# Optimization experiments

Measured on AMD Instinct MI355X. Metric: run time of the kernel, lower is better.

## Reference

```python
import jax, jax.numpy as jnp
import numpy as np

T, H, I, E, TOP_K = 4096, 2048, 768, 16, 2


def _pack_i2s(tern):
    # tern: int8 in {-1,0,1}, shape [..., K] with K % 4 == 0
    m = (tern + 1).astype(jnp.uint8)  # map to {0,1,2}
    m = m.reshape(*tern.shape[:-1], -1, 4)
    return (m[..., 0] | (m[..., 1] << 2) | (m[..., 2] << 4) | (m[..., 3] << 6)).astype(jnp.uint8)


def _quantize_alpha(alpha):
    # per-column alpha -> int8 with global scale (quantize_alpha_int8)
    scale = jnp.maximum(jnp.abs(alpha).max(), 1e-8) / 127.0
    q = jnp.clip(jnp.round(alpha / scale), -128, 127).astype(jnp.int8)
    return q, scale.astype(jnp.float32)


def _unpack_i2s(packed, K, alpha):
    # packed: uint8 [..., N, K//4]; alpha: [..., K] per input column
    shifts = jnp.array([0, 2, 4, 6], dtype=jnp.uint8)
    ext = (packed[..., None] >> shifts) & jnp.uint8(3)  # [..., N, K//4, 4]
    vals = ext.reshape(*packed.shape[:-1], K).astype(jnp.float32) - 1.0  # {-1,0,1}
    return vals * alpha[..., None, :]


def setup_inputs() -> dict:
    key = jax.random.key(0)
    ks = jax.random.split(key, 6)
    x = jax.random.normal(ks[0], (T, H), dtype=jnp.float32)
    router_logits = jax.random.normal(ks[1], (T, E), dtype=jnp.float32)
    tern13 = jax.random.randint(ks[2], (E, 2 * I, H), -1, 2, dtype=jnp.int8)
    tern2 = jax.random.randint(ks[3], (E, H, I), -1, 2, dtype=jnp.int8)
    a13 = jax.random.uniform(ks[4], (E, H), minval=0.01, maxval=0.05, dtype=jnp.float32)
    a2 = jax.random.uniform(ks[5], (E, I), minval=0.01, maxval=0.05, dtype=jnp.float32)
    w13_alpha_q, w13_alpha_scale = _quantize_alpha(a13)
    w2_alpha_q, w2_alpha_scale = _quantize_alpha(a2)
    return {
        "x": x,
        "router_logits": router_logits,
        "w13_packed": _pack_i2s(tern13),
        "w13_alpha_q": w13_alpha_q,
        "w13_alpha_scale": w13_alpha_scale,
        "w2_packed": _pack_i2s(tern2),
        "w2_alpha_q": w2_alpha_q,
        "w2_alpha_scale": w2_alpha_scale,
    }


def reference(x, router_logits, w13_packed, w13_alpha_q, w13_alpha_scale,
              w2_packed, w2_alpha_q, w2_alpha_scale):
    # dequant int8 alphas, then dequant 2-bit ternary weights
    a13 = w13_alpha_q.astype(jnp.float32) * w13_alpha_scale  # [E, H]
    a2 = w2_alpha_q.astype(jnp.float32) * w2_alpha_scale     # [E, I]
    w13 = _unpack_i2s(w13_packed, H, a13)  # [E, 2I, H]
    w2 = _unpack_i2s(w2_packed, I, a2)     # [E, H, I]

    # top-k routing with renormalized softmax weights
    probs = jax.nn.softmax(router_logits, axis=-1)
    topw, topi = jax.lax.top_k(probs, TOP_K)           # [T, k]
    topw = topw / topw.sum(axis=-1, keepdims=True)
    combine = jnp.sum(jax.nn.one_hot(topi, E, dtype=x.dtype) * topw[..., None], axis=1)  # [T, E]

    # grouped expert matmuls (dense dispatch over experts)
    gu = jnp.einsum('th,enh->ten', x, w13)             # [T, E, 2I]
    gate, up = jnp.split(gu, 2, axis=-1)
    act = jax.nn.silu(gate) * up                       # [T, E, I]
    down = jnp.einsum('tei,ehi->teh', act, w2)         # [T, E, H]
    return jnp.einsum('te,teh->th', combine, down)     # [T, H]
```

## Files before the change

### kernel.cpp

```cpp
#include <hip/hip_runtime.h>
#include <stdint.h>

#define T_TOK 4096
#define HDIM  2048
#define IDIM  768
#define NEXP  16
#define NPAIR (T_TOK * 2)
#define PAIR_CAP (NPAIR + 256)

typedef float f32x4 __attribute__((ext_vector_type(4)));
typedef __bf16 bf16x8 __attribute__((ext_vector_type(8)));
typedef unsigned short u16x8 __attribute__((ext_vector_type(8)));
typedef unsigned int u32;
typedef u32 u32x4 __attribute__((ext_vector_type(4)));
typedef const __attribute__((address_space(1))) u32* as1_u32p;
typedef __attribute__((address_space(3))) u32* as3_u32p;

__device__ __forceinline__ unsigned short f2bf(float f) {
  u32 u = __float_as_uint(f);
  u += 0x7FFFu + ((u >> 16) & 1u);
  return (unsigned short)(u >> 16);
}

__device__ __forceinline__ f32x4 mfma16(bf16x8 a, bf16x8 b, f32x4 c) {
  return __builtin_amdgcn_mfma_f32_16x16x32_bf16(a, b, c, 0, 0, 0);
}

__device__ __forceinline__ bf16x8 expand8(u32 w, int qshift) {
  w >>= qshift;
  const u32 t0 = w & 0x03030303u;
  const u32 h0 = __builtin_amdgcn_perm(0u, 0x003F00BFu, t0);
  const u32 l0 = __builtin_amdgcn_perm(0u, 0x00800080u, t0);
  const u32 t1 = (w >> 2) & 0x03030303u;
  const u32 h1 = __builtin_amdgcn_perm(0u, 0x003F00BFu, t1);
  const u32 l1 = __builtin_amdgcn_perm(0u, 0x00800080u, t1);
  u32x4 o;
  o[0] = __builtin_amdgcn_perm(h0, l0, 0x05010400u);
  o[1] = __builtin_amdgcn_perm(h0, l0, 0x07030602u);
  o[2] = __builtin_amdgcn_perm(h1, l1, 0x05010400u);
  o[3] = __builtin_amdgcn_perm(h1, l1, 0x07030602u);
  return __builtin_bit_cast(bf16x8, o);
}

__global__ __launch_bounds__(256) void route_kernel(
    const float* __restrict__ logits, int* __restrict__ counts,
    int* __restrict__ t2i, float* __restrict__ t2w) {
  const int t = blockIdx.x * 256 + threadIdx.x;
  if (t >= T_TOK) return;
  const float* l = logits + t * NEXP;
  float m0 = -1e30f, m1 = -1e30f;
  int i0 = 0, i1 = 0;
#pragma unroll
  for (int j = 0; j < NEXP; ++j) {
    const float v = l[j];
    if (v > m0) { m1 = m0; i1 = i0; m0 = v; i0 = j; }
    else if (v > m1) { m1 = v; i1 = j; }
  }
  const float w0 = 1.0f / (1.0f + expf(m1 - m0));
  t2i[t] = i0 | (i1 << 8);
  t2w[t] = w0;
  atomicAdd(&counts[i0], 1);
  atomicAdd(&counts[i1], 1);
}

__global__ __launch_bounds__(256) void fill_kernel(
    const int* __restrict__ counts, const int* __restrict__ t2i,
    const float* __restrict__ t2w, int* __restrict__ cursor,
    int* __restrict__ offs, int* __restrict__ pair_token,
    float* __restrict__ pair_wt, int* __restrict__ pair_eid) {
  const int t = blockIdx.x * 256 + threadIdx.x;
  if (t >= T_TOK) return;
  const int ii = t2i[t];
  const int i0 = ii & 255, i1 = (ii >> 8) & 255;
  int o0 = 0, o1 = 0, s = 0;
#pragma unroll
  for (int j = 0; j < NEXP; ++j) {
    const int c = counts[j];
    o0 += (j < i0) ? c : 0;
    o1 += (j < i1) ? c : 0;
    s += c;
  }
  if (t == 0) {
    int run = 0;
#pragma unroll
    for (int j = 0; j < NEXP; ++j) { offs[j] = run; run += counts[j]; }
    offs[NEXP] = run;
  }
  const float w0 = t2w[t];
  const int p0 = o0 + atomicAdd(&cursor[i0], 1);
  pair_token[p0] = t; pair_wt[p0] = w0; pair_eid[p0] = i0;
  const int p1 = o1 + atomicAdd(&cursor[i1], 1);
  pair_token[p1] = t; pair_wt[p1] = 1.0f - w0; pair_eid[p1] = i1;
}

#define RP13_BLOCKS 3072
#define RP2_BLOCKS  1536
__global__ __launch_bounds__(256) void repack_kernel(
    const int* __restrict__ w13, u32* __restrict__ o13,
    const int* __restrict__ w2, u32* __restrict__ o2) {
  const int gid = blockIdx.x;
  const int* w;
  u32* o;
  int b;
  if (gid < RP13_BLOCKS) { w = w13; o = o13; b = gid; }
  else                   { w = w2;  o = o2;  b = gid - RP13_BLOCKS; }
  const int j0 = (b * 256 + threadIdx.x) * 4;
  const int4* w4 = (const int4*)w;
  uint4 r;
#pragma unroll
  for (int k = 0; k < 4; ++k) {
    const int4 a = w4[j0 + k];
    u32 x = (u32)(a.x & 255) | ((u32)(a.y & 255) << 8) |
            ((u32)(a.z & 255) << 16) | ((u32)(a.w & 255) << 24);
    u32 t = (x ^ (x >> 12)) & 0x0000F0F0u; x ^= t ^ (t << 12);
    t = (x ^ (x >> 6)) & 0x00CC00CCu;      x ^= t ^ (t << 6);
    ((u32*)&r)[k] = x;
  }
  ((uint4*)o)[b * 256 + threadIdx.x] = r;
}

__global__ __launch_bounds__(256) void xg_kernel(
    const float* __restrict__ x, const int* __restrict__ a13q,
    const float* __restrict__ s13p, const int* __restrict__ pair_token,
    const int* __restrict__ pair_eid, unsigned short* __restrict__ xg) {
  const int p = blockIdx.x;
  const int t = pair_token[p];
  const int e = pair_eid[p];
  const float s13 = *s13p;
  const int h0 = threadIdx.x * 8;
  const float* xp = x + (size_t)t * HDIM + h0;
  const int* ap = a13q + (size_t)e * HDIM + h0;
  const float4 x0 = ((const float4*)xp)[0];
  const float4 x1 = ((const float4*)xp)[1];
  const int4 a0 = ((const int4*)ap)[0];
  const int4 a1 = ((const int4*)ap)[1];
  u16x8 q;
  q[0] = f2bf(x0.x * (float)a0.x * s13);
  q[1] = f2bf(x0.y * (float)a0.y * s13);
  q[2] = f2bf(x0.z * (float)a0.z * s13);
  q[3] = f2bf(x0.w * (float)a0.w * s13);
  q[4] = f2bf(x1.x * (float)a1.x * s13);
  q[5] = f2bf(x1.y * (float)a1.y * s13);
  q[6] = f2bf(x1.z * (float)a1.z * s13);
  q[7] = f2bf(x1.w * (float)a1.w * s13);
  *(u16x8*)(xg + (size_t)p * HDIM + h0) = q;
}

#define DMA_A(src, pitch, dst0, dst1, sidx)                                          \
  {                                                                                  \
    _Pragma("unroll") for (int c = 0; c < 2; ++c) {                                  \
      const unsigned short* gp =                                                     \
          src + (arow0 + wave * 32 + c * 16 + arow) * (pitch) + (sidx) * 64 + acol;  \
      unsigned short* lp = dst0 + (wave * 32 + c * 16) * 32;                         \
      __builtin_amdgcn_global_load_lds((as1_u32p)(const void*)gp,                    \
                                       (as3_u32p)(void*)lp, 16, 0, 0);               \
    }                                                                                \
    _Pragma("unroll") for (int c = 0; c < 2; ++c) {                                  \
      const unsigned short* gp =                                                     \
          src + (arow0 + wave * 32 + c * 16 + arow) * (pitch) + (sidx) * 64 + 32 +   \
          acol;                                                                      \
      unsigned short* lp = dst1 + (wave * 32 + c * 16) * 32;                         \
      __builtin_amdgcn_global_load_lds((as1_u32p)(const void*)gp,                    \
                                       (as3_u32p)(void*)lp, 16, 0, 0);               \
    }                                                                                \
  }

#define DMA_B1(dstq, sidx)                                                           \
  if (wave < 2) {                                                                    \
    const u32* gq = wq13 + ((size_t)e * (2 * IDIM) + wave * IDIM + nT * 64 + lane) * \
                               (HDIM / 16) + (size_t)(sidx) * 4;                     \
    u32* lp = (dstq) + wave * 256;                                                   \
    __builtin_amdgcn_global_load_lds((as1_u32p)(const void*)gq,                      \
                                     (as3_u32p)(void*)lp, 16, 0, 0);                 \
  }

#define DMA_B2(dstq, sidx)                                                           \
  if (wave < 2) {                                                                    \
    const u32* gq = wq2 + ((size_t)e * HDIM + nT * 128 + wave * 64 + lane) *         \
                              (IDIM / 16) + (size_t)(sidx) * 4;                      \
    u32* lp = (dstq) + wave * 256;                                                   \
    __builtin_amdgcn_global_load_lds((as1_u32p)(const void*)gq,                      \
                                     (as3_u32p)(void*)lp, 16, 0, 0);                 \
  }

#define G1_HALF(sAp, sBp, h)                                                        \
  {                                                                                 \
    bf16x8 af[4];                                                                   \
    _Pragma("unroll") for (int mi = 0; mi < 4; ++mi)                                \
        af[mi] = *(const bf16x8*)((sAp) + (wm * 64 + mi * 16 + ln) * 32 + quad * 8);\
    const u32 c0 = (sBp)[(wn * 32 + ln) * 4 + 2 * (h) + qsel];                      \
    const u32 c1 = (sBp)[(wn * 32 + 16 + ln) * 4 + 2 * (h) + qsel];                 \
    const u32 c2 = (sBp)[(64 + wn * 32 + ln) * 4 + 2 * (h) + qsel];                 \
    const u32 c3 = (sBp)[(64 + wn * 32 + 16 + ln) * 4 + 2 * (h) + qsel];            \
    const bf16x8 b0 = expand8(c0, qshift), b1 = expand8(c1, qshift);                \
    const bf16x8 b2 = expand8(c2, qshift), b3 = expand8(c3, qshift);                \
    _Pragma("unroll") for (int mi = 0; mi < 4; ++mi) {                              \
      acc[mi][0] = mfma16(af[mi], b0, acc[mi][0]);                                  \
      acc[mi][1] = mfma16(af[mi], b1, acc[mi][1]);                                  \
      acc[mi][2] = mfma16(af[mi], b2, acc[mi][2]);                                  \
      acc[mi][3] = mfma16(af[mi], b3, acc[mi][3]);                                  \
    }                                                                               \
  }

#define G2_HALF(sAp, sBp, h)                                                        \
  {                                                                                 \
    bf16x8 af[4];                                                                   \
    _Pragma("unroll") for (int mi = 0; mi < 4; ++mi)                                \
        af[mi] = *(const bf16x8*)((sAp) + (wm * 64 + mi * 16 + ln) * 32 + quad * 8);\
    const u32 c0 = (sBp)[(wn * 64 + ln) * 4 + 2 * (h) + qsel];                      \
    const u32 c1 = (sBp)[(wn * 64 + 16 + ln) * 4 + 2 * (h) + qsel];                 \
    const u32 c2 = (sBp)[(wn * 64 + 32 + ln) * 4 + 2 * (h) + qsel];                 \
    const u32 c3 = (sBp)[(wn * 64 + 48 + ln) * 4 + 2 * (h) + qsel];                 \
    const bf16x8 b0 = expand8(c0, qshift), b1 = expand8(c1, qshift);                \
    const bf16x8 b2 = expand8(c2, qshift), b3 = expand8(c3, qshift);                \
    _Pragma("unroll") for (int mi = 0; mi < 4; ++mi) {                              \
      acc[mi][0] = mfma16(af[mi], b0, acc[mi][0]);                                  \
      acc[mi][1] = mfma16(af[mi], b1, acc[mi][1]);                                  \
      acc[mi][2] = mfma16(af[mi], b2, acc[mi][2]);                                  \
      acc[mi][3] = mfma16(af[mi], b3, acc[mi][3]);                                  \
    }                                                                               \
  }

__global__ __launch_bounds__(256, 4) void gemm1_kernel(
    const u32* __restrict__ wq13, const int* __restrict__ a2q,
    const float* __restrict__ s2p, const int* __restrict__ counts,
    const int* __restrict__ offs, const float* __restrict__ pair_wt,
    const unsigned short* __restrict__ xg, unsigned short* __restrict__ act) {
  const int id = blockIdx.x;
  const int xcd = id & 7, sblk = id >> 3;
  const int nT = sblk % 12;
  const int gg = (sblk / 12) * 8 + xcd;
  const int e = gg & 15, mT = gg >> 4;
  const int cnt = counts[e];
  if (mT * 128 >= cnt) return;
  const int base = offs[e];
  const int tid = threadIdx.x;

  __shared__ __align__(16) unsigned short sA[2][2][128 * 32];
  __shared__ __align__(16) u32 sBq[2][512];

  const int wave = tid >> 6, lane = tid & 63;
  const int wm = wave >> 1, wn = wave & 1;
  const int quad = lane >> 4, ln = lane & 15;
  const int qsel = quad >> 1;
  const int qshift = (quad & 1) * 4;

  const int arow = lane >> 2;
  const int acol = (lane & 3) * 8;
  const size_t arow0 = (size_t)(base + mT * 128);

  f32x4 acc[4][4] = {};

  DMA_A(xg, HDIM, sA[0][0], sA[0][1], 0);
  DMA_B1(sBq[0], 0);

  const int NT = HDIM / 64;
  for (int j2 = 0; j2 < NT / 2; ++j2) {
    const int j = 2 * j2;
    __syncthreads();
    DMA_A(xg, HDIM, sA[1][0], sA[1][1], j + 1);
    DMA_B1(sBq[1], j + 1);
    __builtin_amdgcn_s_setprio(1);
    G1_HALF(sA[0][0], sBq[0], 0);
    G1_HALF(sA[0][1], sBq[0], 1);
    __builtin_amdgcn_s_setprio(0);
    __syncthreads();
    if (j2 + 1 < NT / 2) {
      DMA_A(xg, HDIM, sA[0][0], sA[0][1], j + 2);
      DMA_B1(sBq[0], j + 2);
    }
    __builtin_amdgcn_s_setprio(1);
    G1_HALF(sA[1][0], sBq[1], 0);
    G1_HALF(sA[1][1], sBq[1], 1);
    __builtin_amdgcn_s_setprio(0);
  }

  const float s2v = *s2p;
#pragma unroll
  for (int gi = 0; gi < 2; ++gi) {
    const int i = nT * 64 + wn * 32 + gi * 16 + ln;
    const float a2v = (float)a2q[e * IDIM + i] * s2v;
#pragma unroll
    for (int mi = 0; mi < 4; ++mi) {
      const f32x4 g = acc[mi][gi];
      const f32x4 u = acc[mi][gi + 2];
#pragma unroll
      for (int r = 0; r < 4; ++r) {
        const int m = mT * 128 + wm * 64 + mi * 16 + quad * 4 + r;
        if (m < cnt) {
          const float wt = pair_wt[base + m];
          const float gv = g[r];
          const float av = gv / (1.0f + __expf(-gv)) * u[r] * a2v * wt;
          act[(size_t)(base + m) * IDIM + i] = f2bf(av);
        }
      }
    }
  }
}

__global__ __launch_bounds__(256, 4) void gemm2_kernel(
    const u32* __restrict__ wq2, const int* __restrict__ counts,
    const int* __restrict__ offs, const int* __restrict__ pair_token,
    const unsigned short* __restrict__ act, float* __restrict__ out) {
  const int id = blockIdx.x;
  const int xcd = id & 7, sblk = id >> 3;
  const int nT = sblk & 15;
  const int gg = (sblk >> 4) * 8 + xcd;
  const int e = gg & 15, mT = gg >> 4;
  const int cnt = counts[e];
  if (mT * 128 >= cnt) return;
  const int base = offs[e];
  const int tid = threadIdx.x;

  __shared__ __align__(16) unsigned short sA[2][2][128 * 32];
  __shared__ __align__(16) u32 sBq[2][512];

  const int wave = tid >> 6, lane = tid & 63;
  const int wm = wave >> 1, wn = wave & 1;
  const int quad = lane >> 4, ln = lane & 15;
  const int qsel = quad >> 1;
  const int qshift = (quad & 1) * 4;

  const int arow = lane >> 2;
  const int acol = (lane & 3) * 8;
  const size_t arow0 = (size_t)(base + mT * 128);

  f32x4 acc[4][4] = {};

  DMA_A(act, IDIM, sA[0][0], sA[0][1], 0);
  DMA_B2(sBq[0], 0);

  const int NT = IDIM / 64;
  for (int j2 = 0; j2 < NT / 2; ++j2) {
    const int j = 2 * j2;
    __syncthreads();
    DMA_A(act, IDIM, sA[1][0], sA[1][1], j + 1);
    DMA_B2(sBq[1], j + 1);
    __builtin_amdgcn_s_setprio(1);
    G2_HALF(sA[0][0], sBq[0], 0);
    G2_HALF(sA[0][1], sBq[0], 1);
    __builtin_amdgcn_s_setprio(0);
    __syncthreads();
    if (j2 + 1 < NT / 2) {
      DMA_A(act, IDIM, sA[0][0], sA[0][1], j + 2);
      DMA_B2(sBq[0], j + 2);
    }
    __builtin_amdgcn_s_setprio(1);
    G2_HALF(sA[1][0], sBq[1], 0);
    G2_HALF(sA[1][1], sBq[1], 1);
    __builtin_amdgcn_s_setprio(0);
  }

#pragma unroll
  for (int mi = 0; mi < 4; ++mi) {
#pragma unroll
    for (int r = 0; r < 4; ++r) {
      const int ml = wm * 64 + mi * 16 + quad * 4 + r;
      const int m = mT * 128 + ml;
      if (m < cnt) {
        const int tok = pair_token[base + m];
        float* orow = out + (size_t)tok * HDIM + nT * 128 + wn * 64;
#pragma unroll
        for (int ni = 0; ni < 4; ++ni)
          atomicAdd(&orow[ni * 16 + ln], acc[mi][ni][r]);
      }
    }
  }
}

extern "C" void kernel_launch(void* const* d_in, const int* in_sizes, int n_in,
                              void* d_out, int out_size, void* d_ws, size_t ws_size,
                              hipStream_t stream) {
  const float* x      = (const float*)d_in[0];
  const float* logits = (const float*)d_in[1];
  const int*   w13p   = (const int*)d_in[2];
  const int*   a13q   = (const int*)d_in[3];
  const float* s13    = (const float*)d_in[4];
  const int*   w2p    = (const int*)d_in[5];
  const int*   a2q    = (const int*)d_in[6];
  const float* s2     = (const float*)d_in[7];
  float* out = (float*)d_out;

  char* ws = (char*)d_ws;
  int*   counts     = (int*)(ws + 0);
  int*   cursor     = (int*)(ws + 64);
  int*   offs       = (int*)(ws + 128);
  int*   t2i        = (int*)(ws + 256);
  float* t2w        = (float*)(ws + 256 + 4 * T_TOK);
  int*   pair_token = (int*)(ws + 256 + 16 * T_TOK);
  float* pair_wt    = (float*)(ws + 256 + 16 * T_TOK + 4 * PAIR_CAP);
  int*   pair_eid   = (int*)(ws + 256 + 16 * T_TOK + 8 * PAIR_CAP);
  const size_t hdr_end = ((size_t)(256 + 16 * T_TOK + 12 * PAIR_CAP) + 255) & ~(size_t)255;

  const size_t n32_13 = (size_t)NEXP * 2 * IDIM * (HDIM / 16);
  const size_t n32_2  = (size_t)NEXP * HDIM * (IDIM / 16);
  const size_t rp13_b = n32_13 * 4, rp2_b = n32_2 * 4;
  const size_t xg_b   = (size_t)PAIR_CAP * HDIM * 2;

  u32* rp13 = (u32*)(ws + hdr_end);
  u32* rp2  = (u32*)(ws + hdr_end + rp13_b);
  unsigned short* xg  = (unsigned short*)(ws + hdr_end + rp13_b + rp2_b);
  unsigned short* act = (unsigned short*)(ws + hdr_end + rp13_b + rp2_b + xg_b);

  hipMemsetAsync(counts, 0, 256, stream);
  hipMemsetAsync(out, 0, (size_t)T_TOK * HDIM * 4, stream);
  route_kernel<<<T_TOK / 256, 256, 0, stream>>>(logits, counts, t2i, t2w);
  fill_kernel<<<T_TOK / 256, 256, 0, stream>>>(counts, t2i, t2w, cursor, offs,
                                               pair_token, pair_wt, pair_eid);
  repack_kernel<<<RP13_BLOCKS + RP2_BLOCKS, 256, 0, stream>>>(w13p, rp13, w2p, rp2);
  xg_kernel<<<NPAIR, 256, 0, stream>>>(x, a13q, s13, pair_token, pair_eid, xg);

  gemm1_kernel<<<6144, 256, 0, stream>>>(rp13, a2q, s2, counts, offs, pair_wt, xg, act);
  gemm2_kernel<<<8192, 256, 0, stream>>>(rp2, counts, offs, pair_token, act, out);
}
```

Measured before the change: 357.9 us.

## Replace gemm2 atomic scatter with bf16 down buffer and per-token combine kernel

gemm2 now writes each pair's down-projection as bf16 into a per-pair buffer that reuses the xg workspace, and a new combine kernel sums each token's two rows into the fp32 output. This removes the fp32 atomicAdd scatter and the memset of the output. xg_kernel is also reorganised to run per token, reading x once and writing both expert-scaled copies, with token-to-pair indices replacing the pair_token and pair_eid arrays. The cost is an extra kernel launch, an extra round trip through the bf16 down buffer, and bf16 rounding of the partial sums before the combine.

```diff
diff --git a/kernel.cpp b/kernel.cpp
--- a/kernel.cpp
+++ b/kernel.cpp
@@ -66,19 +66,18 @@
 __global__ __launch_bounds__(256) void fill_kernel(
     const int* __restrict__ counts, const int* __restrict__ t2i,
     const float* __restrict__ t2w, int* __restrict__ cursor,
-    int* __restrict__ offs, int* __restrict__ pair_token,
-    float* __restrict__ pair_wt, int* __restrict__ pair_eid) {
+    int* __restrict__ offs, float* __restrict__ pair_wt,
+    int* __restrict__ t2p0, int* __restrict__ t2p1) {
   const int t = blockIdx.x * 256 + threadIdx.x;
   if (t >= T_TOK) return;
   const int ii = t2i[t];
   const int i0 = ii & 255, i1 = (ii >> 8) & 255;
-  int o0 = 0, o1 = 0, s = 0;
+  int o0 = 0, o1 = 0;
 #pragma unroll
   for (int j = 0; j < NEXP; ++j) {
     const int c = counts[j];
     o0 += (j < i0) ? c : 0;
     o1 += (j < i1) ? c : 0;
-    s += c;
   }
   if (t == 0) {
     int run = 0;
@@ -88,9 +87,11 @@
   }
   const float w0 = t2w[t];
   const int p0 = o0 + atomicAdd(&cursor[i0], 1);
-  pair_token[p0] = t; pair_wt[p0] = w0; pair_eid[p0] = i0;
+  pair_wt[p0] = w0;
+  t2p0[t] = p0;
   const int p1 = o1 + atomicAdd(&cursor[i1], 1);
-  pair_token[p1] = t; pair_wt[p1] = 1.0f - w0; pair_eid[p1] = i1;
+  pair_wt[p1] = 1.0f - w0;
+  t2p1[t] = p1;
 }
 
 #define RP13_BLOCKS 3072
@@ -121,29 +122,43 @@
 
 __global__ __launch_bounds__(256) void xg_kernel(
     const float* __restrict__ x, const int* __restrict__ a13q,
-    const float* __restrict__ s13p, const int* __restrict__ pair_token,
-    const int* __restrict__ pair_eid, unsigned short* __restrict__ xg) {
-  const int p = blockIdx.x;
-  const int t = pair_token[p];
-  const int e = pair_eid[p];
+    const float* __restrict__ s13p, const int* __restrict__ t2i,
+    const int* __restrict__ t2p0, const int* __restrict__ t2p1,
+    unsigned short* __restrict__ xg) {
+  const int t = blockIdx.x;
+  const int ii = t2i[t];
+  const int e0 = ii & 255, e1 = (ii >> 8) & 255;
+  const int p0 = t2p0[t], p1 = t2p1[t];
   const float s13 = *s13p;
   const int h0 = threadIdx.x * 8;
   const float* xp = x + (size_t)t * HDIM + h0;
-  const int* ap = a13q + (size_t)e * HDIM + h0;
   const float4 x0 = ((const float4*)xp)[0];
   const float4 x1 = ((const float4*)xp)[1];
-  const int4 a0 = ((const int4*)ap)[0];
-  const int4 a1 = ((const int4*)ap)[1];
-  u16x8 q;
-  q[0] = f2bf(x0.x * (float)a0.x * s13);
-  q[1] = f2bf(x0.y * (float)a0.y * s13);
-  q[2] = f2bf(x0.z * (float)a0.z * s13);
-  q[3] = f2bf(x0.w * (float)a0.w * s13);
-  q[4] = f2bf(x1.x * (float)a1.x * s13);
-  q[5] = f2bf(x1.y * (float)a1.y * s13);
-  q[6] = f2bf(x1.z * (float)a1.z * s13);
-  q[7] = f2bf(x1.w * (float)a1.w * s13);
-  *(u16x8*)(xg + (size_t)p * HDIM + h0) = q;
+  const int* ap0 = a13q + (size_t)e0 * HDIM + h0;
+  const int* ap1 = a13q + (size_t)e1 * HDIM + h0;
+  const int4 a00 = ((const int4*)ap0)[0];
+  const int4 a01 = ((const int4*)ap0)[1];
+  const int4 a10 = ((const int4*)ap1)[0];
+  const int4 a11 = ((const int4*)ap1)[1];
+  u16x8 q0, q1;
+  q0[0] = f2bf(x0.x * (float)a00.x * s13);
+  q0[1] = f2bf(x0.y * (float)a00.y * s13);
+  q0[2] = f2bf(x0.z * (float)a00.z * s13);
+  q0[3] = f2bf(x0.w * (float)a00.w * s13);
+  q0[4] = f2bf(x1.x * (float)a01.x * s13);
+  q0[5] = f2bf(x1.y * (float)a01.y * s13);
+  q0[6] = f2bf(x1.z * (float)a01.z * s13);
+  q0[7] = f2bf(x1.w * (float)a01.w * s13);
+  q1[0] = f2bf(x0.x * (float)a10.x * s13);
+  q1[1] = f2bf(x0.y * (float)a10.y * s13);
+  q1[2] = f2bf(x0.z * (float)a10.z * s13);
+  q1[3] = f2bf(x0.w * (float)a10.w * s13);
+  q1[4] = f2bf(x1.x * (float)a11.x * s13);
+  q1[5] = f2bf(x1.y * (float)a11.y * s13);
+  q1[6] = f2bf(x1.z * (float)a11.z * s13);
+  q1[7] = f2bf(x1.w * (float)a11.w * s13);
+  *(u16x8*)(xg + (size_t)p0 * HDIM + h0) = q0;
+  *(u16x8*)(xg + (size_t)p1 * HDIM + h0) = q1;
 }
 
 #define DMA_A(src, pitch, dst0, dst1, sidx)                                          \
@@ -300,8 +315,8 @@
 
 __global__ __launch_bounds__(256, 4) void gemm2_kernel(
     const u32* __restrict__ wq2, const int* __restrict__ counts,
-    const int* __restrict__ offs, const int* __restrict__ pair_token,
-    const unsigned short* __restrict__ act, float* __restrict__ out) {
+    const int* __restrict__ offs, const unsigned short* __restrict__ act,
+    unsigned short* __restrict__ down) {
   const int id = blockIdx.x;
   const int xcd = id & 7, sblk = id >> 3;
   const int nT = sblk & 15;
@@ -358,14 +373,31 @@
       const int ml = wm * 64 + mi * 16 + quad * 4 + r;
       const int m = mT * 128 + ml;
       if (m < cnt) {
-        const int tok = pair_token[base + m];
-        float* orow = out + (size_t)tok * HDIM + nT * 128 + wn * 64;
+        unsigned short* drow = down + (size_t)(base + m) * HDIM + nT * 128 + wn * 64;
 #pragma unroll
         for (int ni = 0; ni < 4; ++ni)
-          atomicAdd(&orow[ni * 16 + ln], acc[mi][ni][r]);
+          drow[ni * 16 + ln] = f2bf(acc[mi][ni][r]);
       }
     }
   }
+}
+
+__global__ __launch_bounds__(256) void combine_kernel(
+    const int* __restrict__ t2p0, const int* __restrict__ t2p1,
+    const unsigned short* __restrict__ down, float* __restrict__ out) {
+  const int t = blockIdx.x;
+  const int h = threadIdx.x * 8;
+  const u16x8 a = *(const u16x8*)(down + (size_t)t2p0[t] * HDIM + h);
+  const u16x8 b = *(const u16x8*)(down + (size_t)t2p1[t] * HDIM + h);
+  f32x4 o0, o1;
+#pragma unroll
+  for (int j = 0; j < 4; ++j) {
+    o0[j] = __uint_as_float((u32)a[j] << 16) + __uint_as_float((u32)b[j] << 16);
+    o1[j] = __uint_as_float((u32)a[j + 4] << 16) + __uint_as_float((u32)b[j + 4] << 16);
+  }
+  float* o = out + (size_t)t * HDIM + h;
+  *(f32x4*)(o) = o0;
+  *(f32x4*)(o + 4) = o1;
 }
 
 extern "C" void kernel_launch(void* const* d_in, const int* in_sizes, int n_in,
@@ -387,10 +419,10 @@
   int*   offs       = (int*)(ws + 128);
   int*   t2i        = (int*)(ws + 256);
   float* t2w        = (float*)(ws + 256 + 4 * T_TOK);
-  int*   pair_token = (int*)(ws + 256 + 16 * T_TOK);
-  float* pair_wt    = (float*)(ws + 256 + 16 * T_TOK + 4 * PAIR_CAP);
-  int*   pair_eid   = (int*)(ws + 256 + 16 * T_TOK + 8 * PAIR_CAP);
-  const size_t hdr_end = ((size_t)(256 + 16 * T_TOK + 12 * PAIR_CAP) + 255) & ~(size_t)255;
+  int*   t2p0       = (int*)(ws + 256 + 8 * T_TOK);
+  int*   t2p1       = (int*)(ws + 256 + 12 * T_TOK);
+  float* pair_wt    = (float*)(ws + 256 + 16 * T_TOK);
+  const size_t hdr_end = ((size_t)(256 + 16 * T_TOK + 4 * PAIR_CAP) + 255) & ~(size_t)255;
 
   const size_t n32_13 = (size_t)NEXP * 2 * IDIM * (HDIM / 16);
   const size_t n32_2  = (size_t)NEXP * HDIM * (IDIM / 16);
@@ -401,15 +433,16 @@
   u32* rp2  = (u32*)(ws + hdr_end + rp13_b);
   unsigned short* xg  = (unsigned short*)(ws + hdr_end + rp13_b + rp2_b);
   unsigned short* act = (unsigned short*)(ws + hdr_end + rp13_b + rp2_b + xg_b);
+  unsigned short* down = xg;
 
   hipMemsetAsync(counts, 0, 256, stream);
-  hipMemsetAsync(out, 0, (size_t)T_TOK * HDIM * 4, stream);
   route_kernel<<<T_TOK / 256, 256, 0, stream>>>(logits, counts, t2i, t2w);
   fill_kernel<<<T_TOK / 256, 256, 0, stream>>>(counts, t2i, t2w, cursor, offs,
-                                               pair_token, pair_wt, pair_eid);
+                                               pair_wt, t2p0, t2p1);
   repack_kernel<<<RP13_BLOCKS + RP2_BLOCKS, 256, 0, stream>>>(w13p, rp13, w2p, rp2);
-  xg_kernel<<<NPAIR, 256, 0, stream>>>(x, a13q, s13, pair_token, pair_eid, xg);
+  xg_kernel<<<T_TOK, 256, 0, stream>>>(x, a13q, s13, t2i, t2p0, t2p1, xg);
 
   gemm1_kernel<<<6144, 256, 0, stream>>>(rp13, a2q, s2, counts, offs, pair_wt, xg, act);
-  gemm2_kernel<<<8192, 256, 0, stream>>>(rp2, counts, offs, pair_token, act, out);
-}
+  gemm2_kernel<<<8192, 256, 0, stream>>>(rp2, counts, offs, act, down);
+  combine_kernel<<<T_TOK, 256, 0, stream>>>(t2p0, t2p1, down, out);
+}
```

New measurement: 328.6 us. -8.2%, faster.
